# Performance work log

Hardware: AMD Instinct MI355X
Metric: run time of the kernel (lower is better)

The kernel has to match this reference:

```python
import jax, jax.numpy as jnp
import numpy as np
from math import gamma, comb

D_POLY = 4
OFFSET = 2
EVAL_MAX = 1.4
N_NODES = 50000
N_EDGES = 800000
IN_FEATS = 256
H_FEATS = 64
NEG_SLOPE = 0.01  # F.leaky_relu / nn.LeakyReLU default


def _beta(a, b):
    return gamma(a) * gamma(b) / gamma(a + b)


def _calculate_theta2(d=D_POLY):
    # Closed-form expansion of sympy poly in calculate_theta2:
    # f(x) = (x/e)^i * (1 - x/e)^(d-i+offset) / (e * Beta(i+1, d+1-i+offset))
    # Returns ascending-order coefficient lists (theta[k] = coeff of x^k).
    e = EVAL_MAX
    thetas = []
    for i in range(OFFSET, d + 1 + OFFSET):
        m = d - i + OFFSET
        B = _beta(i + 1, d + 1 - i + OFFSET)
        c = np.zeros(d + 1 + OFFSET, dtype=np.float64)
        for j in range(m + 1):
            c[i + j] = (1.0 / e) ** i * comb(m, j) * (-1.0 / e) ** j / (e * B)
        thetas.append([float(v) for v in c])
    return thetas


THETAS = _calculate_theta2()


def setup_inputs() -> dict:
    key = jax.random.key(0)
    k1, k2, k3, k4, k5 = jax.random.split(key, 5)
    x = jax.random.normal(k1, (N_NODES, IN_FEATS), dtype=jnp.float32)
    W = jax.random.normal(k2, (IN_FEATS, H_FEATS), dtype=jnp.float32) * 0.05
    b = jax.random.normal(k3, (H_FEATS,), dtype=jnp.float32) * 0.05
    src = jax.random.randint(k4, (N_EDGES,), 0, N_NODES, dtype=jnp.int32)
    dst = jax.random.randint(k5, (N_EDGES,), 0, N_NODES, dtype=jnp.int32)
    return {"x": x, "W": W, "b": b, "src": src, "dst": dst}


def reference(x, W, b, src, dst):
    # BWGNN forward: linear + LeakyReLU, then 5 Beta-wavelet PolyConv filters.
    h = jax.nn.leaky_relu(x @ W + b, NEG_SLOPE)  # [N, H]
    # out_degrees, clamped to 1, then D^{-1/2}
    deg = jax.ops.segment_sum(jnp.ones_like(src, dtype=h.dtype), src, num_segments=N_NODES)
    d_inv = jnp.clip(deg, 1.0) ** -0.5
    d_inv = d_inv[:, None]  # [N, 1]
    outs = []
    for theta in THETAS:
        f = h
        acc = theta[0] * h
        for k in range(1, len(theta)):
            # unnLaplacian: f <- f - D^{-1/2} A^T D^{-1/2} f  (copy_u/sum SpMM)
            msg = jax.ops.segment_sum((f * d_inv)[src], dst, num_segments=N_NODES)
            f = f - msg * d_inv
            acc = acc + theta[k] * f
        outs.append(acc)
    return jnp.concatenate(outs, axis=1)  # [N, 5*H]
```

## Files before the change

kernel.cpp:

```cpp
#include <hip/hip_runtime.h>
#include <math.h>

#define NN 50000
#define NN4 12500
#define NE 800000
#define INF 256
#define HF 64
#define OUTF 320
#define NB4 ((NN4 + 255) / 256)
#define G 128
#define SL (NE / G)

typedef _Float16 half8 __attribute__((ext_vector_type(8)));
typedef float floatx4 __attribute__((ext_vector_type(4)));
typedef float f32x2 __attribute__((ext_vector_type(2)));
typedef float f32x4 __attribute__((ext_vector_type(4)));

static __device__ __forceinline__ unsigned short f2h(float x) {
    _Float16 h = (_Float16)x;
    return *(unsigned short*)&h;
}
static __device__ __forceinline__ float h2f(unsigned short u) {
    _Float16 h = *(_Float16*)&u;
    return (float)h;
}

struct ThetaM { float m[5][7]; };

static void compute_theta(ThetaM& tm) {
    const double e = 1.4;
    auto fact = [](int n) { double r = 1.0; for (int i = 2; i <= n; ++i) r *= i; return r; };
    for (int t = 0; t < 5; ++t) {
        int i = t + 2;
        int mm = 6 - i;
        double B = fact(i) * fact(6 - i) / fact(7);
        for (int k = 0; k < 7; ++k) tm.m[t][k] = 0.f;
        for (int j = 0; j <= mm; ++j) {
            double cb = fact(mm) / (fact(j) * fact(mm - j));
            double v = pow(1.0 / e, (double)i) * cb * pow(-1.0 / e, (double)j) / (e * B);
            tm.m[t][i + j] = (float)v;
        }
    }
}

__global__ __launch_bounds__(1024) void hist_kernel(const int* __restrict__ src,
                                                    const int* __restrict__ dst,
                                                    unsigned int* __restrict__ hist_dst,
                                                    unsigned int* __restrict__ hist_src,
                                                    unsigned int* __restrict__ gA,
                                                    unsigned int* __restrict__ gB) {
    __shared__ unsigned int h[NN4];
    int b = blockIdx.x;
    if (b == 0 && threadIdx.x < 32) gA[NN * 32 + threadIdx.x] = 0u;
    if (b == 1 && threadIdx.x < 32) gB[NN * 32 + threadIdx.x] = 0u;
    const int* arr = (b < G) ? dst : src;
    unsigned int* outp = (b < G) ? hist_dst : hist_src;
    int bb = (b < G) ? b : b - G;
    for (int i = threadIdx.x; i < NN4; i += 1024) h[i] = 0u;
    __syncthreads();
    int base = bb * SL;
    for (int i = threadIdx.x; i < SL; i += 1024) {
        int d = arr[base + i];
        atomicAdd(&h[d >> 2], 1u << ((d & 3) * 8));
    }
    __syncthreads();
    unsigned int* out32 = outp + (size_t)bb * NN4;
    for (int i = threadIdx.x; i < NN4; i += 1024) out32[i] = h[i];
}

__global__ __launch_bounds__(256) void merge_kernel(unsigned int* __restrict__ hist_dst,
                                                    const unsigned int* __restrict__ hist_src,
                                                    int* __restrict__ cnt,
                                                    float* __restrict__ dinv,
                                                    int* __restrict__ partial) {
    __shared__ int s[256];
    int tid = threadIdx.x;
    int t = blockIdx.x * 256 + tid;
    int run0 = 0, run1 = 0, run2 = 0, run3 = 0;
    if (t < NN4) {
        for (int b = 0; b < G; ++b) {
            size_t idx = (size_t)b * NN4 + t;
            unsigned int u = hist_dst[idx];
            hist_dst[idx] = (unsigned int)run0 | ((unsigned int)run1 << 8) |
                            ((unsigned int)run2 << 16) | ((unsigned int)run3 << 24);
            run0 += u & 255u; run1 += (u >> 8) & 255u;
            run2 += (u >> 16) & 255u; run3 += u >> 24;
        }
        *(int4*)&cnt[4 * t] = make_int4(run0, run1, run2, run3);
        int d0 = 0, d1 = 0, d2 = 0, d3 = 0;
        for (int b = 0; b < G; ++b) {
            unsigned int u = hist_src[(size_t)b * NN4 + t];
            d0 += u & 255u; d1 += (u >> 8) & 255u;
            d2 += (u >> 16) & 255u; d3 += u >> 24;
        }
        float e0 = (float)(d0 < 1 ? 1 : d0);
        float e1 = (float)(d1 < 1 ? 1 : d1);
        float e2 = (float)(d2 < 1 ? 1 : d2);
        float e3 = (float)(d3 < 1 ? 1 : d3);
        *(float4*)&dinv[4 * t] = make_float4(1.0f / sqrtf(e0), 1.0f / sqrtf(e1),
                                             1.0f / sqrtf(e2), 1.0f / sqrtf(e3));
    }
    int pad = ((run0 + 7) & ~7) + ((run1 + 7) & ~7) + ((run2 + 7) & ~7) + ((run3 + 7) & ~7);
    s[tid] = pad;
    __syncthreads();
    for (int off = 128; off > 0; off >>= 1) {
        if (tid < off) s[tid] += s[tid + off];
        __syncthreads();
    }
    if (tid == 0) partial[blockIdx.x] = s[0];
}

__global__ __launch_bounds__(256) void scan_partials_kernel(const int* __restrict__ partial,
                                                            int* __restrict__ offsets,
                                                            int* __restrict__ row_ptr) {
    __shared__ int s[256];
    int tid = threadIdx.x;
    s[tid] = (tid < NB4) ? partial[tid] : 0;
    __syncthreads();
    for (int off = 1; off < 256; off <<= 1) {
        int t = (tid >= off) ? s[tid - off] : 0;
        __syncthreads();
        s[tid] += t;
        __syncthreads();
    }
    if (tid < NB4) offsets[tid] = (tid == 0) ? 0 : s[tid - 1];
    if (tid == NB4 - 1) row_ptr[NN] = s[tid];
}

__global__ __launch_bounds__(256) void scan_write_kernel(const int* __restrict__ cnt,
                                                         const int* __restrict__ offsets,
                                                         int* __restrict__ row_ptr,
                                                         int* __restrict__ col) {
    __shared__ int s[256];
    int tid = threadIdx.x;
    int t = blockIdx.x * 256 + tid;
    int4 c = make_int4(0, 0, 0, 0);
    if (t < NN4) c = *(const int4*)&cnt[4 * t];
    int p0 = (c.x + 7) & ~7, p1 = (c.y + 7) & ~7, p2 = (c.z + 7) & ~7, p3 = (c.w + 7) & ~7;
    int csum = p0 + p1 + p2 + p3;
    s[tid] = csum;
    __syncthreads();
    for (int off = 1; off < 256; off <<= 1) {
        int v = (tid >= off) ? s[tid - off] : 0;
        __syncthreads();
        s[tid] += v;
        __syncthreads();
    }
    if (t < NN4) {
        int b0 = offsets[blockIdx.x] + s[tid] - csum;
        int b1 = b0 + p0, b2 = b1 + p1, b3 = b2 + p2;
        *(int4*)&row_ptr[4 * t] = make_int4(b0, b1, b2, b3);
        const int PH = NN << 5;
        for (int k = c.x; k < p0; ++k) col[b0 + k] = PH;
        for (int k = c.y; k < p1; ++k) col[b1 + k] = PH;
        for (int k = c.z; k < p2; ++k) col[b2 + k] = PH;
        for (int k = c.w; k < p3; ++k) col[b3 + k] = PH;
    }
}

__global__ __launch_bounds__(1024) void fill_kernel(const int* __restrict__ src,
                                                    const int* __restrict__ dst,
                                                    const unsigned char* __restrict__ hist8,
                                                    const int* __restrict__ row_ptr,
                                                    int* __restrict__ col) {
    __shared__ unsigned int cur[NN4];
    int b = blockIdx.x;
    for (int i = threadIdx.x; i < NN4; i += 1024) cur[i] = 0u;
    __syncthreads();
    int base = b * SL;
    const unsigned char* hrow = hist8 + (size_t)b * NN;
    for (int i = threadIdx.x; i < SL; i += 1024) {
        int d = dst[base + i];
        int sh = (d & 3) * 8;
        unsigned int old = atomicAdd(&cur[d >> 2], 1u << sh);
        int rank = (int)((old >> sh) & 255u);
        int pos = row_ptr[d] + (int)hrow[d] + rank;
        col[pos] = src[base + i] << 5;
    }
}

__global__ __launch_bounds__(256) void wprep_kernel(const float* __restrict__ W,
                                                    unsigned short* __restrict__ Wt) {
    int id = blockIdx.x * 256 + threadIdx.x;
    if (id >= HF * INF) return;
    int n = id >> 8;
    int k = id & 255;
    Wt[id] = f2h(W[k * HF + n]);
}

__global__ __launch_bounds__(256) void gemm_kernel(const float* __restrict__ x,
                                                   const unsigned short* __restrict__ Wt,
                                                   const float* __restrict__ b,
                                                   const float* __restrict__ dinv,
                                                   float* __restrict__ f,
                                                   unsigned short* __restrict__ g) {
    __shared__ _Float16 wls[64 * 264];
    __shared__ _Float16 xls[64 * 136];
    int tid = threadIdx.x;
    int row0 = blockIdx.x * 64;
    int wave = tid >> 6;
    int lane = tid & 63;
    int q = lane >> 4;
    int ln = lane & 15;

    {
        const uint4* wg = (const uint4*)Wt;
        for (int i = 0; i < 8; ++i) {
            int l = tid + i * 256;
            int r = l >> 5, c = l & 31;
            *(uint4*)&wls[r * 264 + c * 8] = wg[l];
        }
    }

    floatx4 acc[4] = {{0.f,0.f,0.f,0.f},{0.f,0.f,0.f,0.f},{0.f,0.f,0.f,0.f},{0.f,0.f,0.f,0.f}};

    for (int ch = 0; ch < 2; ++ch) {
        __syncthreads();
        for (int i = 0; i < 8; ++i) {
            int l = tid + i * 256;
            int r = l >> 5, c4 = (l & 31) * 4;
            int grow = row0 + r;
            f32x4 v = {0.f, 0.f, 0.f, 0.f};
            if (grow < NN) v = __builtin_nontemporal_load((const f32x4*)&x[(size_t)grow * INF + ch * 128 + c4]);
            ushort4 hv;
            hv.x = f2h(v[0]); hv.y = f2h(v[1]); hv.z = f2h(v[2]); hv.w = f2h(v[3]);
            *(ushort4*)&xls[r * 136 + c4] = hv;
        }
        __syncthreads();
        int m = wave * 16 + ln;
        #pragma unroll
        for (int kb4 = 0; kb4 < 4; ++kb4) {
            int kb = kb4 * 32;
            half8 a = *(const half8*)&xls[m * 136 + kb + q * 8];
            int kg = ch * 128 + kb + q * 8;
            #pragma unroll
            for (int t = 0; t < 4; ++t) {
                half8 bb = *(const half8*)&wls[(t * 16 + ln) * 264 + kg];
                acc[t] = __builtin_amdgcn_mfma_f32_16x16x32_f16(a, bb, acc[t], 0, 0, 0);
            }
        }
    }

    float bias[4];
    #pragma unroll
    for (int t = 0; t < 4; ++t) bias[t] = b[t * 16 + ln];
    #pragma unroll
    for (int r = 0; r < 4; ++r) {
        int grow = row0 + wave * 16 + q * 4 + r;
        if (grow < NN) {
            float dv = dinv[grow];
            #pragma unroll
            for (int t = 0; t < 4; ++t) {
                float h = acc[t][r] + bias[t];
                h = (h > 0.f) ? h : 0.01f * h;
                int cidx = t * 16 + ln;
                f[(size_t)grow * HF + cidx] = h;
                g[(size_t)grow * HF + cidx] = f2h(h * dv);
            }
        }
    }
}

#define ACC8(ca, cb)                                                           \
    do {                                                                       \
        unsigned int u0 = g_in[(unsigned)(ca.x + c2)];                         \
        unsigned int u1 = g_in[(unsigned)(ca.y + c2)];                         \
        unsigned int u2 = g_in[(unsigned)(ca.z + c2)];                         \
        unsigned int u3 = g_in[(unsigned)(ca.w + c2)];                         \
        unsigned int u4 = g_in[(unsigned)(cb.x + c2)];                         \
        unsigned int u5 = g_in[(unsigned)(cb.y + c2)];                         \
        unsigned int u6 = g_in[(unsigned)(cb.z + c2)];                         \
        unsigned int u7 = g_in[(unsigned)(cb.w + c2)];                         \
        s0 += ((h2f(u0 & 0xFFFF) + h2f(u1 & 0xFFFF)) + (h2f(u2 & 0xFFFF) + h2f(u3 & 0xFFFF)))  \
            + ((h2f(u4 & 0xFFFF) + h2f(u5 & 0xFFFF)) + (h2f(u6 & 0xFFFF) + h2f(u7 & 0xFFFF))); \
        s1 += ((h2f(u0 >> 16) + h2f(u1 >> 16)) + (h2f(u2 >> 16) + h2f(u3 >> 16)))              \
            + ((h2f(u4 >> 16) + h2f(u5 >> 16)) + (h2f(u6 >> 16) + h2f(u7 >> 16)));             \
    } while (0)

__global__ __launch_bounds__(256) void prop_kernel(const int* __restrict__ row_ptr,
                                                   const int* __restrict__ col,
                                                   const float* __restrict__ dinv,
                                                   const unsigned int* __restrict__ g_in,
                                                   const float* __restrict__ f_in, int fin_stride,
                                                   float* __restrict__ f_out, int fout_stride,
                                                   unsigned int* __restrict__ g_out) {
    int gidx = blockIdx.x * 256 + threadIdx.x;
    int wid = gidx >> 5;
    int c2 = threadIdx.x & 31;
    if (wid >= NN) return;
    int j   = row_ptr[wid];
    int end = row_ptr[wid + 1];
    float dv = dinv[wid];
    f32x2 fv = __builtin_nontemporal_load((const f32x2*)&f_in[(size_t)wid * fin_stride + 2 * c2]);
    float s0 = 0.f, s1 = 0.f;
    if (j < end) {
        const int4* c4p = (const int4*)(col + j);
        int nit = (end - j) >> 3;
        int4 ca = c4p[0], cb = c4p[1];
        c4p += 2;
        for (int it = 1; it < nit; ++it) {
            int4 na = c4p[0], nb = c4p[1];
            c4p += 2;
            ACC8(ca, cb);
            ca = na; cb = nb;
        }
        ACC8(ca, cb);
    }
    float fx = fv[0] - s0 * dv;
    float fy = fv[1] - s1 * dv;
    f32x2 ov; ov[0] = fx; ov[1] = fy;
    __builtin_nontemporal_store(ov, (f32x2*)&f_out[(size_t)wid * fout_stride + 2 * c2]);
    if (g_out) g_out[wid * 32 + c2] = (unsigned int)f2h(fx * dv) | ((unsigned int)f2h(fy * dv) << 16);
}

__global__ __launch_bounds__(256) void prop_final_kernel(const int* __restrict__ row_ptr,
                                                         const int* __restrict__ col,
                                                         const float* __restrict__ dinv,
                                                         const unsigned int* __restrict__ g_in,
                                                         float* __restrict__ out, ThetaM tm) {
    int gidx = blockIdx.x * 256 + threadIdx.x;
    int wid = gidx >> 5;
    int c2 = threadIdx.x & 31;
    if (wid >= NN) return;
    int j   = row_ptr[wid];
    int end = row_ptr[wid + 1];
    float dv = dinv[wid];
    float* orow = out + (size_t)wid * OUTF + 2 * c2;
    f32x2 v2 = *(const f32x2*)&orow[0 * HF];
    f32x2 v3 = *(const f32x2*)&orow[1 * HF];
    f32x2 v4 = *(const f32x2*)&orow[2 * HF];
    f32x2 v5 = *(const f32x2*)&orow[3 * HF];
    float s0 = 0.f, s1 = 0.f;
    if (j < end) {
        const int4* c4p = (const int4*)(col + j);
        int nit = (end - j) >> 3;
        int4 ca = c4p[0], cb = c4p[1];
        c4p += 2;
        for (int it = 1; it < nit; ++it) {
            int4 na = c4p[0], nb = c4p[1];
            c4p += 2;
            ACC8(ca, cb);
            ca = na; cb = nb;
        }
        ACC8(ca, cb);
    }
    f32x2 v6; v6[0] = v5[0] - s0 * dv; v6[1] = v5[1] - s1 * dv;
    f32x2 v[5] = {v2, v3, v4, v5, v6};
    #pragma unroll
    for (int t = 0; t < 5; ++t) {
        f32x2 o = {0.f, 0.f};
        #pragma unroll
        for (int jj = 0; jj < 5; ++jj) {
            if (jj >= t) { o[0] += tm.m[t][jj + 2] * v[jj][0]; o[1] += tm.m[t][jj + 2] * v[jj][1]; }
        }
        __builtin_nontemporal_store(o, (f32x2*)&orow[t * HF]);
    }
}

extern "C" void kernel_launch(void* const* d_in, const int* in_sizes, int n_in,
                              void* d_out, int out_size, void* d_ws, size_t ws_size,
                              hipStream_t stream) {
    const float* x  = (const float*)d_in[0];
    const float* W  = (const float*)d_in[1];
    const float* b  = (const float*)d_in[2];
    const int* src  = (const int*)d_in[3];
    const int* dst  = (const int*)d_in[4];
    float* out = (float*)d_out;

    char* ws = (char*)d_ws;
    size_t off = 0;
    auto alloc = [&](size_t bytes) -> void* {
        void* p = ws + off;
        off += (bytes + 255) & ~(size_t)255;
        return p;
    };
    unsigned int* hist_dst = (unsigned int*)alloc((size_t)G * NN4 * 4);
    unsigned int* hist_src = (unsigned int*)alloc((size_t)G * NN4 * 4);
    int*   cnt     = (int*)alloc((size_t)NN * 4);
    int*   row_ptr = (int*)alloc((size_t)(NN + 1) * 4);
    int*   partial = (int*)alloc((size_t)NB4 * 4);
    int*   offsets = (int*)alloc((size_t)NB4 * 4);
    float* dinv    = (float*)alloc((size_t)NN * 4);
    int*   col     = (int*)alloc((size_t)(NE + 8 * NN) * 4);
    unsigned short* wt = (unsigned short*)alloc((size_t)HF * INF * 2);
    float* fbuf    = (float*)alloc((size_t)NN * HF * 4);
    unsigned short* gA = (unsigned short*)alloc((size_t)(NN + 1) * HF * 2);
    unsigned short* gB = (unsigned short*)alloc((size_t)(NN + 1) * HF * 2);

    hist_kernel<<<2 * G, 1024, 0, stream>>>(src, dst, hist_dst, hist_src,
                                            (unsigned int*)gA, (unsigned int*)gB);
    merge_kernel<<<NB4, 256, 0, stream>>>(hist_dst, hist_src, cnt, dinv, partial);
    scan_partials_kernel<<<1, 256, 0, stream>>>(partial, offsets, row_ptr);
    scan_write_kernel<<<NB4, 256, 0, stream>>>(cnt, offsets, row_ptr, col);
    fill_kernel<<<G, 1024, 0, stream>>>(src, dst, (const unsigned char*)hist_dst, row_ptr, col);
    wprep_kernel<<<(HF * INF + 255) / 256, 256, 0, stream>>>(W, wt);
    gemm_kernel<<<(NN + 63) / 64, 256, 0, stream>>>(x, wt, b, dinv, fbuf, gA);

    ThetaM tm;
    compute_theta(tm);

    const int PB = (NN * 32 + 255) / 256;
    prop_kernel<<<PB, 256, 0, stream>>>(row_ptr, col, dinv, (unsigned int*)gA, fbuf, HF, fbuf, HF, (unsigned int*)gB);
    prop_kernel<<<PB, 256, 0, stream>>>(row_ptr, col, dinv, (unsigned int*)gB, fbuf, HF, out + 0 * HF, OUTF, (unsigned int*)gA);
    prop_kernel<<<PB, 256, 0, stream>>>(row_ptr, col, dinv, (unsigned int*)gA, out + 0 * HF, OUTF, out + 1 * HF, OUTF, (unsigned int*)gB);
    prop_kernel<<<PB, 256, 0, stream>>>(row_ptr, col, dinv, (unsigned int*)gB, out + 1 * HF, OUTF, out + 2 * HF, OUTF, (unsigned int*)gA);
    prop_kernel<<<PB, 256, 0, stream>>>(row_ptr, col, dinv, (unsigned int*)gA, out + 2 * HF, OUTF, out + 3 * HF, OUTF, (unsigned int*)gB);
    prop_final_kernel<<<PB, 256, 0, stream>>>(row_ptr, col, dinv, (unsigned int*)gB, out, tm);
}
```

Measured before the change: 302.3 us.

## Use full 64-lane waves per node with 16-byte gathers and shuffle reduction

The SpMM propagation kernels now assign one 64-lane wavefront per node. Each group of 8 lanes handles one edge and gathers 16 bytes (8 half values) per lane, replacing the 32-lane layout where each lane read 4 bytes per edge. Partial sums are combined with xor-shuffles across edge groups, and a quarter of the lanes then write 4-wide outputs. This aims for wider memory transactions and fewer load instructions, at the cost of twice the threads, eight accumulators per lane and a shuffle reduction. The fill kernel also switches its column write to a nontemporal store.

```diff
diff --git a/kernel.cpp b/kernel.cpp
--- a/kernel.cpp
+++ b/kernel.cpp
@@ -175,7 +175,7 @@
         unsigned int old = atomicAdd(&cur[d >> 2], 1u << sh);
         int rank = (int)((old >> sh) & 255u);
         int pos = row_ptr[d] + (int)hrow[d] + rank;
-        col[pos] = src[base + i] << 5;
+        __builtin_nontemporal_store(src[base + i] << 5, &col[pos]);
     }
 }
 
@@ -261,21 +261,12 @@
     }
 }
 
-#define ACC8(ca, cb)                                                           \
-    do {                                                                       \
-        unsigned int u0 = g_in[(unsigned)(ca.x + c2)];                         \
-        unsigned int u1 = g_in[(unsigned)(ca.y + c2)];                         \
-        unsigned int u2 = g_in[(unsigned)(ca.z + c2)];                         \
-        unsigned int u3 = g_in[(unsigned)(ca.w + c2)];                         \
-        unsigned int u4 = g_in[(unsigned)(cb.x + c2)];                         \
-        unsigned int u5 = g_in[(unsigned)(cb.y + c2)];                         \
-        unsigned int u6 = g_in[(unsigned)(cb.z + c2)];                         \
-        unsigned int u7 = g_in[(unsigned)(cb.w + c2)];                         \
-        s0 += ((h2f(u0 & 0xFFFF) + h2f(u1 & 0xFFFF)) + (h2f(u2 & 0xFFFF) + h2f(u3 & 0xFFFF)))  \
-            + ((h2f(u4 & 0xFFFF) + h2f(u5 & 0xFFFF)) + (h2f(u6 & 0xFFFF) + h2f(u7 & 0xFFFF))); \
-        s1 += ((h2f(u0 >> 16) + h2f(u1 >> 16)) + (h2f(u2 >> 16) + h2f(u3 >> 16)))              \
-            + ((h2f(u4 >> 16) + h2f(u5 >> 16)) + (h2f(u6 >> 16) + h2f(u7 >> 16)));             \
-    } while (0)
+static __device__ __forceinline__ void acc8(float* s, uint4 u) {
+    s[0] += h2f(u.x & 0xFFFF); s[1] += h2f(u.x >> 16);
+    s[2] += h2f(u.y & 0xFFFF); s[3] += h2f(u.y >> 16);
+    s[4] += h2f(u.z & 0xFFFF); s[5] += h2f(u.z >> 16);
+    s[6] += h2f(u.w & 0xFFFF); s[7] += h2f(u.w >> 16);
+}
 
 __global__ __launch_bounds__(256) void prop_kernel(const int* __restrict__ row_ptr,
                                                    const int* __restrict__ col,
@@ -285,32 +276,46 @@
                                                    float* __restrict__ f_out, int fout_stride,
                                                    unsigned int* __restrict__ g_out) {
     int gidx = blockIdx.x * 256 + threadIdx.x;
-    int wid = gidx >> 5;
-    int c2 = threadIdx.x & 31;
+    int wid = gidx >> 6;
     if (wid >= NN) return;
+    int lane = threadIdx.x & 63;
+    int e = lane >> 3;
+    int c = lane & 7;
     int j   = row_ptr[wid];
     int end = row_ptr[wid + 1];
     float dv = dinv[wid];
-    f32x2 fv = __builtin_nontemporal_load((const f32x2*)&f_in[(size_t)wid * fin_stride + 2 * c2]);
-    float s0 = 0.f, s1 = 0.f;
+    float s[8] = {0.f, 0.f, 0.f, 0.f, 0.f, 0.f, 0.f, 0.f};
     if (j < end) {
-        const int4* c4p = (const int4*)(col + j);
         int nit = (end - j) >> 3;
-        int4 ca = c4p[0], cb = c4p[1];
-        c4p += 2;
+        unsigned cv = (unsigned)col[j + e] + c * 4;
         for (int it = 1; it < nit; ++it) {
-            int4 na = c4p[0], nb = c4p[1];
-            c4p += 2;
-            ACC8(ca, cb);
-            ca = na; cb = nb;
-        }
-        ACC8(ca, cb);
-    }
-    float fx = fv[0] - s0 * dv;
-    float fy = fv[1] - s1 * dv;
-    f32x2 ov; ov[0] = fx; ov[1] = fy;
-    __builtin_nontemporal_store(ov, (f32x2*)&f_out[(size_t)wid * fout_stride + 2 * c2]);
-    if (g_out) g_out[wid * 32 + c2] = (unsigned int)f2h(fx * dv) | ((unsigned int)f2h(fy * dv) << 16);
+            unsigned cn = (unsigned)col[j + it * 8 + e] + c * 4;
+            uint4 u = *(const uint4*)&g_in[cv];
+            acc8(s, u);
+            cv = cn;
+        }
+        uint4 u = *(const uint4*)&g_in[cv];
+        acc8(s, u);
+    }
+    #pragma unroll
+    for (int off = 8; off <= 32; off <<= 1) {
+        #pragma unroll
+        for (int k = 0; k < 8; ++k) s[k] += __shfl_xor(s[k], off, 64);
+    }
+    if (e < 2) {
+        int fo = c * 8 + e * 4;
+        f32x4 fv = __builtin_nontemporal_load((const f32x4*)&f_in[(size_t)wid * fin_stride + fo]);
+        f32x4 ox;
+        #pragma unroll
+        for (int k = 0; k < 4; ++k) ox[k] = fv[k] - s[e * 4 + k] * dv;
+        __builtin_nontemporal_store(ox, (f32x4*)&f_out[(size_t)wid * fout_stride + fo]);
+        if (g_out) {
+            uint2 gw;
+            gw.x = (unsigned)f2h(ox[0] * dv) | ((unsigned)f2h(ox[1] * dv) << 16);
+            gw.y = (unsigned)f2h(ox[2] * dv) | ((unsigned)f2h(ox[3] * dv) << 16);
+            *(uint2*)&g_out[wid * 32 + c * 4 + e * 2] = gw;
+        }
+    }
 }
 
 __global__ __launch_bounds__(256) void prop_final_kernel(const int* __restrict__ row_ptr,
@@ -319,41 +324,53 @@
                                                          const unsigned int* __restrict__ g_in,
                                                          float* __restrict__ out, ThetaM tm) {
     int gidx = blockIdx.x * 256 + threadIdx.x;
-    int wid = gidx >> 5;
-    int c2 = threadIdx.x & 31;
+    int wid = gidx >> 6;
     if (wid >= NN) return;
+    int lane = threadIdx.x & 63;
+    int e = lane >> 3;
+    int c = lane & 7;
     int j   = row_ptr[wid];
     int end = row_ptr[wid + 1];
     float dv = dinv[wid];
-    float* orow = out + (size_t)wid * OUTF + 2 * c2;
-    f32x2 v2 = *(const f32x2*)&orow[0 * HF];
-    f32x2 v3 = *(const f32x2*)&orow[1 * HF];
-    f32x2 v4 = *(const f32x2*)&orow[2 * HF];
-    f32x2 v5 = *(const f32x2*)&orow[3 * HF];
-    float s0 = 0.f, s1 = 0.f;
+    float s[8] = {0.f, 0.f, 0.f, 0.f, 0.f, 0.f, 0.f, 0.f};
     if (j < end) {
-        const int4* c4p = (const int4*)(col + j);
         int nit = (end - j) >> 3;
-        int4 ca = c4p[0], cb = c4p[1];
-        c4p += 2;
+        unsigned cv = (unsigned)col[j + e] + c * 4;
         for (int it = 1; it < nit; ++it) {
-            int4 na = c4p[0], nb = c4p[1];
-            c4p += 2;
-            ACC8(ca, cb);
-            ca = na; cb = nb;
-        }
-        ACC8(ca, cb);
-    }
-    f32x2 v6; v6[0] = v5[0] - s0 * dv; v6[1] = v5[1] - s1 * dv;
-    f32x2 v[5] = {v2, v3, v4, v5, v6};
+            unsigned cn = (unsigned)col[j + it * 8 + e] + c * 4;
+            uint4 u = *(const uint4*)&g_in[cv];
+            acc8(s, u);
+            cv = cn;
+        }
+        uint4 u = *(const uint4*)&g_in[cv];
+        acc8(s, u);
+    }
     #pragma unroll
-    for (int t = 0; t < 5; ++t) {
-        f32x2 o = {0.f, 0.f};
-        #pragma unroll
-        for (int jj = 0; jj < 5; ++jj) {
-            if (jj >= t) { o[0] += tm.m[t][jj + 2] * v[jj][0]; o[1] += tm.m[t][jj + 2] * v[jj][1]; }
-        }
-        __builtin_nontemporal_store(o, (f32x2*)&orow[t * HF]);
+    for (int off = 8; off <= 32; off <<= 1) {
+        #pragma unroll
+        for (int k = 0; k < 8; ++k) s[k] += __shfl_xor(s[k], off, 64);
+    }
+    if (e < 2) {
+        float* orow = out + (size_t)wid * OUTF + c * 8 + e * 4;
+        f32x4 v[5];
+        v[0] = *(const f32x4*)&orow[0 * HF];
+        v[1] = *(const f32x4*)&orow[1 * HF];
+        v[2] = *(const f32x4*)&orow[2 * HF];
+        v[3] = *(const f32x4*)&orow[3 * HF];
+        #pragma unroll
+        for (int k = 0; k < 4; ++k) v[4][k] = v[3][k] - s[e * 4 + k] * dv;
+        #pragma unroll
+        for (int t = 0; t < 5; ++t) {
+            f32x4 o = {0.f, 0.f, 0.f, 0.f};
+            #pragma unroll
+            for (int jj = 0; jj < 5; ++jj) {
+                if (jj >= t) {
+                    #pragma unroll
+                    for (int k = 0; k < 4; ++k) o[k] += tm.m[t][jj + 2] * v[jj][k];
+                }
+            }
+            __builtin_nontemporal_store(o, (f32x4*)&orow[t * HF]);
+        }
     }
 }
 
@@ -399,7 +416,7 @@
     ThetaM tm;
     compute_theta(tm);
 
-    const int PB = (NN * 32 + 255) / 256;
+    const int PB = (NN * 64) / 256;
     prop_kernel<<<PB, 256, 0, stream>>>(row_ptr, col, dinv, (unsigned int*)gA, fbuf, HF, fbuf, HF, (unsigned int*)gB);
     prop_kernel<<<PB, 256, 0, stream>>>(row_ptr, col, dinv, (unsigned int*)gB, fbuf, HF, out + 0 * HF, OUTF, (unsigned int*)gA);
     prop_kernel<<<PB, 256, 0, stream>>>(row_ptr, col, dinv, (unsigned int*)gA, out + 0 * HF, OUTF, out + 1 * HF, OUTF, (unsigned int*)gB);
```

Measured after the change: 353.4 us. +16.9%, slower.

## Replace block-local rank CSR fill with global atomic cursor scatter

Applied to the files above, without the earlier changes.

The CSR fill phase no longer writes per-block exclusive prefix counts back into the histogram in merge, nor uses per-block LDS atomics with a byte rank lookup. Instead scan_write initializes a per-node cursor array from row_ptr, and a fully parallel fill kernel does one global atomicAdd per edge to claim a slot, storing with nontemporal writes. This removes the 128-pass read-modify-write of hist_dst and the large-LDS 128-block fill, trading them for contended global atomics and a non-deterministic edge order within each row.

```diff
diff --git a/kernel.cpp b/kernel.cpp
--- a/kernel.cpp
+++ b/kernel.cpp
@@ -68,7 +68,7 @@
     for (int i = threadIdx.x; i < NN4; i += 1024) out32[i] = h[i];
 }
 
-__global__ __launch_bounds__(256) void merge_kernel(unsigned int* __restrict__ hist_dst,
+__global__ __launch_bounds__(256) void merge_kernel(const unsigned int* __restrict__ hist_dst,
                                                     const unsigned int* __restrict__ hist_src,
                                                     int* __restrict__ cnt,
                                                     float* __restrict__ dinv,
@@ -79,10 +79,7 @@
     int run0 = 0, run1 = 0, run2 = 0, run3 = 0;
     if (t < NN4) {
         for (int b = 0; b < G; ++b) {
-            size_t idx = (size_t)b * NN4 + t;
-            unsigned int u = hist_dst[idx];
-            hist_dst[idx] = (unsigned int)run0 | ((unsigned int)run1 << 8) |
-                            ((unsigned int)run2 << 16) | ((unsigned int)run3 << 24);
+            unsigned int u = hist_dst[(size_t)b * NN4 + t];
             run0 += u & 255u; run1 += (u >> 8) & 255u;
             run2 += (u >> 16) & 255u; run3 += u >> 24;
         }
@@ -130,6 +127,7 @@
 __global__ __launch_bounds__(256) void scan_write_kernel(const int* __restrict__ cnt,
                                                          const int* __restrict__ offsets,
                                                          int* __restrict__ row_ptr,
+                                                         int* __restrict__ cursor,
                                                          int* __restrict__ col) {
     __shared__ int s[256];
     int tid = threadIdx.x;
@@ -150,6 +148,7 @@
         int b0 = offsets[blockIdx.x] + s[tid] - csum;
         int b1 = b0 + p0, b2 = b1 + p1, b3 = b2 + p2;
         *(int4*)&row_ptr[4 * t] = make_int4(b0, b1, b2, b3);
+        *(int4*)&cursor[4 * t]  = make_int4(b0, b1, b2, b3);
         const int PH = NN << 5;
         for (int k = c.x; k < p0; ++k) col[b0 + k] = PH;
         for (int k = c.y; k < p1; ++k) col[b1 + k] = PH;
@@ -158,25 +157,15 @@
     }
 }
 
-__global__ __launch_bounds__(1024) void fill_kernel(const int* __restrict__ src,
-                                                    const int* __restrict__ dst,
-                                                    const unsigned char* __restrict__ hist8,
-                                                    const int* __restrict__ row_ptr,
-                                                    int* __restrict__ col) {
-    __shared__ unsigned int cur[NN4];
-    int b = blockIdx.x;
-    for (int i = threadIdx.x; i < NN4; i += 1024) cur[i] = 0u;
-    __syncthreads();
-    int base = b * SL;
-    const unsigned char* hrow = hist8 + (size_t)b * NN;
-    for (int i = threadIdx.x; i < SL; i += 1024) {
-        int d = dst[base + i];
-        int sh = (d & 3) * 8;
-        unsigned int old = atomicAdd(&cur[d >> 2], 1u << sh);
-        int rank = (int)((old >> sh) & 255u);
-        int pos = row_ptr[d] + (int)hrow[d] + rank;
-        col[pos] = src[base + i] << 5;
-    }
+__global__ __launch_bounds__(256) void fill_kernel(const int* __restrict__ src,
+                                                   const int* __restrict__ dst,
+                                                   int* __restrict__ cursor,
+                                                   int* __restrict__ col) {
+    int i = blockIdx.x * 256 + threadIdx.x;
+    if (i >= NE) return;
+    int d = dst[i];
+    int pos = atomicAdd(&cursor[d], 1);
+    __builtin_nontemporal_store(src[i] << 5, &col[pos]);
 }
 
 __global__ __launch_bounds__(256) void wprep_kernel(const float* __restrict__ W,
@@ -378,6 +367,7 @@
     unsigned int* hist_src = (unsigned int*)alloc((size_t)G * NN4 * 4);
     int*   cnt     = (int*)alloc((size_t)NN * 4);
     int*   row_ptr = (int*)alloc((size_t)(NN + 1) * 4);
+    int*   cursor  = (int*)alloc((size_t)NN * 4);
     int*   partial = (int*)alloc((size_t)NB4 * 4);
     int*   offsets = (int*)alloc((size_t)NB4 * 4);
     float* dinv    = (float*)alloc((size_t)NN * 4);
@@ -391,8 +381,8 @@
                                             (unsigned int*)gA, (unsigned int*)gB);
     merge_kernel<<<NB4, 256, 0, stream>>>(hist_dst, hist_src, cnt, dinv, partial);
     scan_partials_kernel<<<1, 256, 0, stream>>>(partial, offsets, row_ptr);
-    scan_write_kernel<<<NB4, 256, 0, stream>>>(cnt, offsets, row_ptr, col);
-    fill_kernel<<<G, 1024, 0, stream>>>(src, dst, (const unsigned char*)hist_dst, row_ptr, col);
+    scan_write_kernel<<<NB4, 256, 0, stream>>>(cnt, offsets, row_ptr, cursor, col);
+    fill_kernel<<<(NE + 255) / 256, 256, 0, stream>>>(src, dst, cursor, col);
     wprep_kernel<<<(HF * INF + 255) / 256, 256, 0, stream>>>(W, wt);
     gemm_kernel<<<(NN + 63) / 64, 256, 0, stream>>>(x, wt, b, dinv, fbuf, gA);
 
```

Measured after the change: 329.0 us. 1.09x slower.

## Split propagation features into two 32-column halves to shrink gather working set

Applied to the files above, without the earlier changes.

Splits the fp16 scaled feature buffers into separate low and high 32-column arrays and runs the full six-step propagation chain twice, once per half, with 16 lanes per node instead of 32. The gathered g array per pass halves, so it is more likely to fit in cache during the random gathers. In exchange, the CSR column indices are read twice as often, and twice as many kernels are launched. The fill kernel's column stores also become nontemporal.

```diff
diff --git a/kernel.cpp b/kernel.cpp
--- a/kernel.cpp
+++ b/kernel.cpp
@@ -47,12 +47,16 @@
                                                     const int* __restrict__ dst,
                                                     unsigned int* __restrict__ hist_dst,
                                                     unsigned int* __restrict__ hist_src,
-                                                    unsigned int* __restrict__ gA,
-                                                    unsigned int* __restrict__ gB) {
+                                                    unsigned int* __restrict__ gAlo,
+                                                    unsigned int* __restrict__ gAhi,
+                                                    unsigned int* __restrict__ gBlo,
+                                                    unsigned int* __restrict__ gBhi) {
     __shared__ unsigned int h[NN4];
     int b = blockIdx.x;
-    if (b == 0 && threadIdx.x < 32) gA[NN * 32 + threadIdx.x] = 0u;
-    if (b == 1 && threadIdx.x < 32) gB[NN * 32 + threadIdx.x] = 0u;
+    if (b == 0 && threadIdx.x < 16) gAlo[NN * 16 + threadIdx.x] = 0u;
+    if (b == 1 && threadIdx.x < 16) gAhi[NN * 16 + threadIdx.x] = 0u;
+    if (b == 2 && threadIdx.x < 16) gBlo[NN * 16 + threadIdx.x] = 0u;
+    if (b == 3 && threadIdx.x < 16) gBhi[NN * 16 + threadIdx.x] = 0u;
     const int* arr = (b < G) ? dst : src;
     unsigned int* outp = (b < G) ? hist_dst : hist_src;
     int bb = (b < G) ? b : b - G;
@@ -150,7 +154,7 @@
         int b0 = offsets[blockIdx.x] + s[tid] - csum;
         int b1 = b0 + p0, b2 = b1 + p1, b3 = b2 + p2;
         *(int4*)&row_ptr[4 * t] = make_int4(b0, b1, b2, b3);
-        const int PH = NN << 5;
+        const int PH = NN << 4;
         for (int k = c.x; k < p0; ++k) col[b0 + k] = PH;
         for (int k = c.y; k < p1; ++k) col[b1 + k] = PH;
         for (int k = c.z; k < p2; ++k) col[b2 + k] = PH;
@@ -175,7 +179,7 @@
         unsigned int old = atomicAdd(&cur[d >> 2], 1u << sh);
         int rank = (int)((old >> sh) & 255u);
         int pos = row_ptr[d] + (int)hrow[d] + rank;
-        col[pos] = src[base + i] << 5;
+        __builtin_nontemporal_store(src[base + i] << 4, &col[pos]);
     }
 }
 
@@ -193,7 +197,8 @@
                                                    const float* __restrict__ b,
                                                    const float* __restrict__ dinv,
                                                    float* __restrict__ f,
-                                                   unsigned short* __restrict__ g) {
+                                                   unsigned short* __restrict__ g_lo,
+                                                   unsigned short* __restrict__ g_hi) {
     __shared__ _Float16 wls[64 * 264];
     __shared__ _Float16 xls[64 * 136];
     int tid = threadIdx.x;
@@ -255,7 +260,9 @@
                 h = (h > 0.f) ? h : 0.01f * h;
                 int cidx = t * 16 + ln;
                 f[(size_t)grow * HF + cidx] = h;
-                g[(size_t)grow * HF + cidx] = f2h(h * dv);
+                unsigned short gv = f2h(h * dv);
+                if (t < 2) g_lo[grow * 32 + cidx] = gv;
+                else       g_hi[grow * 32 + (cidx - 32)] = gv;
             }
         }
     }
@@ -283,15 +290,17 @@
                                                    const unsigned int* __restrict__ g_in,
                                                    const float* __restrict__ f_in, int fin_stride,
                                                    float* __restrict__ f_out, int fout_stride,
-                                                   unsigned int* __restrict__ g_out) {
+                                                   unsigned int* __restrict__ g_out,
+                                                   int phase) {
     int gidx = blockIdx.x * 256 + threadIdx.x;
-    int wid = gidx >> 5;
-    int c2 = threadIdx.x & 31;
+    int wid = gidx >> 4;
+    int c2 = threadIdx.x & 15;
     if (wid >= NN) return;
     int j   = row_ptr[wid];
     int end = row_ptr[wid + 1];
     float dv = dinv[wid];
-    f32x2 fv = __builtin_nontemporal_load((const f32x2*)&f_in[(size_t)wid * fin_stride + 2 * c2]);
+    int fo = phase * 32 + c2 * 2;
+    f32x2 fv = __builtin_nontemporal_load((const f32x2*)&f_in[(size_t)wid * fin_stride + fo]);
     float s0 = 0.f, s1 = 0.f;
     if (j < end) {
         const int4* c4p = (const int4*)(col + j);
@@ -309,23 +318,24 @@
     float fx = fv[0] - s0 * dv;
     float fy = fv[1] - s1 * dv;
     f32x2 ov; ov[0] = fx; ov[1] = fy;
-    __builtin_nontemporal_store(ov, (f32x2*)&f_out[(size_t)wid * fout_stride + 2 * c2]);
-    if (g_out) g_out[wid * 32 + c2] = (unsigned int)f2h(fx * dv) | ((unsigned int)f2h(fy * dv) << 16);
+    __builtin_nontemporal_store(ov, (f32x2*)&f_out[(size_t)wid * fout_stride + fo]);
+    if (g_out) g_out[wid * 16 + c2] = (unsigned int)f2h(fx * dv) | ((unsigned int)f2h(fy * dv) << 16);
 }
 
 __global__ __launch_bounds__(256) void prop_final_kernel(const int* __restrict__ row_ptr,
                                                          const int* __restrict__ col,
                                                          const float* __restrict__ dinv,
                                                          const unsigned int* __restrict__ g_in,
-                                                         float* __restrict__ out, ThetaM tm) {
+                                                         float* __restrict__ out, ThetaM tm,
+                                                         int phase) {
     int gidx = blockIdx.x * 256 + threadIdx.x;
-    int wid = gidx >> 5;
-    int c2 = threadIdx.x & 31;
+    int wid = gidx >> 4;
+    int c2 = threadIdx.x & 15;
     if (wid >= NN) return;
     int j   = row_ptr[wid];
     int end = row_ptr[wid + 1];
     float dv = dinv[wid];
-    float* orow = out + (size_t)wid * OUTF + 2 * c2;
+    float* orow = out + (size_t)wid * OUTF + phase * 32 + c2 * 2;
     f32x2 v2 = *(const f32x2*)&orow[0 * HF];
     f32x2 v3 = *(const f32x2*)&orow[1 * HF];
     f32x2 v4 = *(const f32x2*)&orow[2 * HF];
@@ -384,26 +394,47 @@
     int*   col     = (int*)alloc((size_t)(NE + 8 * NN) * 4);
     unsigned short* wt = (unsigned short*)alloc((size_t)HF * INF * 2);
     float* fbuf    = (float*)alloc((size_t)NN * HF * 4);
-    unsigned short* gA = (unsigned short*)alloc((size_t)(NN + 1) * HF * 2);
-    unsigned short* gB = (unsigned short*)alloc((size_t)(NN + 1) * HF * 2);
+    unsigned short* gAlo = (unsigned short*)alloc((size_t)(NN + 1) * 32 * 2);
+    unsigned short* gAhi = (unsigned short*)alloc((size_t)(NN + 1) * 32 * 2);
+    unsigned short* gBlo = (unsigned short*)alloc((size_t)(NN + 1) * 32 * 2);
+    unsigned short* gBhi = (unsigned short*)alloc((size_t)(NN + 1) * 32 * 2);
 
     hist_kernel<<<2 * G, 1024, 0, stream>>>(src, dst, hist_dst, hist_src,
-                                            (unsigned int*)gA, (unsigned int*)gB);
+                                            (unsigned int*)gAlo, (unsigned int*)gAhi,
+                                            (unsigned int*)gBlo, (unsigned int*)gBhi);
     merge_kernel<<<NB4, 256, 0, stream>>>(hist_dst, hist_src, cnt, dinv, partial);
     scan_partials_kernel<<<1, 256, 0, stream>>>(partial, offsets, row_ptr);
     scan_write_kernel<<<NB4, 256, 0, stream>>>(cnt, offsets, row_ptr, col);
     fill_kernel<<<G, 1024, 0, stream>>>(src, dst, (const unsigned char*)hist_dst, row_ptr, col);
     wprep_kernel<<<(HF * INF + 255) / 256, 256, 0, stream>>>(W, wt);
-    gemm_kernel<<<(NN + 63) / 64, 256, 0, stream>>>(x, wt, b, dinv, fbuf, gA);
+    gemm_kernel<<<(NN + 63) / 64, 256, 0, stream>>>(x, wt, b, dinv, fbuf, gAlo, gBhi ? gAhi : gAhi);
 
     ThetaM tm;
     compute_theta(tm);
 
-    const int PB = (NN * 32 + 255) / 256;
-    prop_kernel<<<PB, 256, 0, stream>>>(row_ptr, col, dinv, (unsigned int*)gA, fbuf, HF, fbuf, HF, (unsigned int*)gB);
-    prop_kernel<<<PB, 256, 0, stream>>>(row_ptr, col, dinv, (unsigned int*)gB, fbuf, HF, out + 0 * HF, OUTF, (unsigned int*)gA);
-    prop_kernel<<<PB, 256, 0, stream>>>(row_ptr, col, dinv, (unsigned int*)gA, out + 0 * HF, OUTF, out + 1 * HF, OUTF, (unsigned int*)gB);
-    prop_kernel<<<PB, 256, 0, stream>>>(row_ptr, col, dinv, (unsigned int*)gB, out + 1 * HF, OUTF, out + 2 * HF, OUTF, (unsigned int*)gA);
-    prop_kernel<<<PB, 256, 0, stream>>>(row_ptr, col, dinv, (unsigned int*)gA, out + 2 * HF, OUTF, out + 3 * HF, OUTF, (unsigned int*)gB);
-    prop_final_kernel<<<PB, 256, 0, stream>>>(row_ptr, col, dinv, (unsigned int*)gB, out, tm);
-}
+    const int PB = (NN * 16) / 256;
+
+    prop_kernel<<<PB, 256, 0, stream>>>(row_ptr, col, dinv, (unsigned int*)gAlo,
+                                        fbuf, HF, fbuf, HF, (unsigned int*)gBlo, 0);
+    prop_kernel<<<PB, 256, 0, stream>>>(row_ptr, col, dinv, (unsigned int*)gBlo,
+                                        fbuf, HF, out + 0 * HF, OUTF, (unsigned int*)gAlo, 0);
+    prop_kernel<<<PB, 256, 0, stream>>>(row_ptr, col, dinv, (unsigned int*)gAlo,
+                                        out + 0 * HF, OUTF, out + 1 * HF, OUTF, (unsigned int*)gBlo, 0);
+    prop_kernel<<<PB, 256, 0, stream>>>(row_ptr, col, dinv, (unsigned int*)gBlo,
+                                        out + 1 * HF, OUTF, out + 2 * HF, OUTF, (unsigned int*)gAlo, 0);
+    prop_kernel<<<PB, 256, 0, stream>>>(row_ptr, col, dinv, (unsigned int*)gAlo,
+                                        out + 2 * HF, OUTF, out + 3 * HF, OUTF, (unsigned int*)gBlo, 0);
+    prop_final_kernel<<<PB, 256, 0, stream>>>(row_ptr, col, dinv, (unsigned int*)gBlo, out, tm, 0);
+
+    prop_kernel<<<PB, 256, 0, stream>>>(row_ptr, col, dinv, (unsigned int*)gAhi,
+                                        fbuf, HF, fbuf, HF, (unsigned int*)gBhi, 1);
+    prop_kernel<<<PB, 256, 0, stream>>>(row_ptr, col, dinv, (unsigned int*)gBhi,
+                                        fbuf, HF, out + 0 * HF, OUTF, (unsigned int*)gAhi, 1);
+    prop_kernel<<<PB, 256, 0, stream>>>(row_ptr, col, dinv, (unsigned int*)gAhi,
+                                        out + 0 * HF, OUTF, out + 1 * HF, OUTF, (unsigned int*)gBhi, 1);
+    prop_kernel<<<PB, 256, 0, stream>>>(row_ptr, col, dinv, (unsigned int*)gBhi,
+                                        out + 1 * HF, OUTF, out + 2 * HF, OUTF, (unsigned int*)gAhi, 1);
+    prop_kernel<<<PB, 256, 0, stream>>>(row_ptr, col, dinv, (unsigned int*)gAhi,
+                                        out + 2 * HF, OUTF, out + 3 * HF, OUTF, (unsigned int*)gBhi, 1);
+    prop_final_kernel<<<PB, 256, 0, stream>>>(row_ptr, col, dinv, (unsigned int*)gBhi, out, tm, 1);
+}
```

Measured after the change: 345.0 us. 1.14x slower.
